# Performance work log

Hardware: AMD Instinct MI355X
Metric: run time of the kernel (lower is better)

The kernel has to match this reference:

```python
import jax, jax.numpy as jnp
import numpy as np

B, BOND, N, ATOM, UNITS = 256, 5, 128, 64, 128


def setup_inputs() -> dict:
    key = jax.random.key(0)
    k1, k2, k3 = jax.random.split(key, 3)
    adjacency = jax.random.uniform(k1, (B, BOND, N, N), dtype=jnp.float32)
    features = jax.random.normal(k2, (B, N, ATOM), dtype=jnp.float32)
    # per-sample unique kernel: (global_batch, bond_dim, atom_dim, units)
    kernel = jax.random.normal(k3, (B, BOND, ATOM, UNITS), dtype=jnp.float32) * 0.05
    return {"adjacency": adjacency, "features": features, "kernel": kernel}


def reference(adjacency, features, kernel):
    # aggregate neighbors per bond type: [B, bond, N, atom]
    x = jnp.einsum('bemn,bnd->bemd', adjacency, features)
    # per-sample, per-bond linear transform: [B, bond, N, units]
    x = jnp.einsum('bemd,bedu->bemu', x, kernel)
    # reduce over bond types, then activation: [B, N, units]
    return jax.nn.relu(jnp.sum(x, axis=1))
```

## Files before the change

### kernel.cpp

```cpp
#include <hip/hip_runtime.h>


typedef __attribute__((ext_vector_type(8))) short s8v;
typedef __attribute__((ext_vector_type(4))) float f4v;

__device__ __forceinline__ unsigned bfr(float f) {
    unsigned u = __builtin_bit_cast(unsigned, f);
    u += 0x7FFFu + ((u >> 16) & 1u);
    return u >> 16;
}
__device__ __forceinline__ unsigned pk2(float a, float b) {
    return bfr(a) | (bfr(b) << 16);
}
__device__ __forceinline__ s8v mk_frag(f4v lo, f4v hi) {
    union { unsigned u[4]; s8v s; } r;
    r.u[0] = pk2(lo[0], lo[1]); r.u[1] = pk2(lo[2], lo[3]);
    r.u[2] = pk2(hi[0], hi[1]); r.u[3] = pk2(hi[2], hi[3]);
    return r.s;
}
__device__ __forceinline__ int adrF(int d, int n) {
    return d * 128 + (((n >> 3) ^ (d & 7)) << 3) + (n & 7);
}
__device__ __forceinline__ int adrK(int u, int d) {
    return u * 64 + (((d >> 3) ^ (u & 7)) << 3) + (d & 7);
}

__global__ __launch_bounds__(256, 4)
void rgc_kernel(const float* __restrict__ adj,
                const float* __restrict__ feat,
                const float* __restrict__ ker,
                float* __restrict__ out)
{
    __shared__ __align__(16) short featT[64 * 128];
    __shared__ __align__(16) short kerT[128 * 64];
    __shared__ __align__(16) short YB[4][16 * 64];

    const int bs   = blockIdx.x & 255;
    const int Q    = blockIdx.x >> 8;
    const int tid  = threadIdx.x;
    const int w    = tid >> 6;
    const int mt   = w >> 1;
    const int uh   = w & 1;
    const int lane = tid & 63;
    const int c16  = lane & 15;
    const int quad = lane >> 4;

    const float* adjB  = adj  + (size_t)bs * (5 * 128 * 128);
    const float* featB = feat + (size_t)bs * (128 * 64);
    const float* kerB  = ker  + (size_t)bs * (5 * 64 * 128);
    float*       outB  = out  + (size_t)bs * (128 * 128);

    {
        const int sn = tid & 127, sdh = tid >> 7;
        const float* fp = featB + sn * 64 + sdh * 32;
        f4v v[8];
        #pragma unroll
        for (int i = 0; i < 8; ++i) v[i] = *(const f4v*)(fp + 4 * i);
        #pragma unroll
        for (int i = 0; i < 8; ++i)
            #pragma unroll
            for (int j = 0; j < 4; ++j) {
                const int d = 32 * sdh + 4 * i + j;
                featT[adrF(d, sn)] = (short)bfr(v[i][j]);
            }
    }
    {
        const float* kp = kerB + lane * 128 + 32 * w;
        f4v v[8];
        #pragma unroll
        for (int i = 0; i < 8; ++i) v[i] = *(const f4v*)(kp + 4 * i);
        #pragma unroll
        for (int i = 0; i < 8; ++i)
            #pragma unroll
            for (int j = 0; j < 4; ++j) {
                const int u = 32 * w + 4 * i + j;
                kerT[adrK(u, lane)] = (short)bfr(v[i][j]);
            }
    }
    __syncthreads();

    const int rowS = 32 * Q + 16 * mt;
    const float* ap0 = adjB + (rowS + c16) * 128 + 8 * quad;
    short* YBw = YB[w];

    f4v oacc[4] = {};

    for (int e = 0; e < 5; ++e) {
        const float* ap = ap0 + e * 16384;
        f4v a0[4], a1[4];
        #pragma unroll
        for (int k16 = 0; k16 < 4; ++k16) {
            a0[k16] = *(const f4v*)(ap + 32 * k16);
            a1[k16] = *(const f4v*)(ap + 32 * k16 + 4);
        }
        f4v kv[8];
        if (e < 4) {
            const float* kp = kerB + (e + 1) * 8192 + lane * 128 + 32 * w;
            #pragma unroll
            for (int i = 0; i < 8; ++i) kv[i] = *(const f4v*)(kp + 4 * i);
        }

        f4v yacc[4] = {};
        #pragma unroll
        for (int k16 = 0; k16 < 4; ++k16) {
            s8v af = mk_frag(a0[k16], a1[k16]);
            #pragma unroll
            for (int d16 = 0; d16 < 4; ++d16) {
                const int d = 16 * d16 + c16;
                s8v bf = *(const s8v*)&featT[d * 128 + (((4 * k16 + quad) ^ (d & 7)) << 3)];
                yacc[d16] = __builtin_amdgcn_mfma_f32_16x16x32_bf16(af, bf, yacc[d16], 0, 0, 0);
            }
        }

        #pragma unroll
        for (int d16 = 0; d16 < 4; ++d16)
            #pragma unroll
            for (int r = 0; r < 4; ++r) {
                const int m = 4 * quad + r;
                YBw[adrK(m, 16 * d16 + c16)] = (short)bfr(yacc[d16][r]);
            }
        s8v y0 = *(const s8v*)&YBw[c16 * 64 + ((quad ^ (c16 & 7)) << 3)];
        s8v y1 = *(const s8v*)&YBw[c16 * 64 + (((4 + quad) ^ (c16 & 7)) << 3)];

        #pragma unroll
        for (int u16 = 0; u16 < 4; ++u16) {
            const int uc = 64 * uh + 16 * u16 + c16;
            s8v b0 = *(const s8v*)&kerT[uc * 64 + ((quad ^ (uc & 7)) << 3)];
            s8v b1 = *(const s8v*)&kerT[uc * 64 + (((4 + quad) ^ (uc & 7)) << 3)];
            oacc[u16] = __builtin_amdgcn_mfma_f32_16x16x32_bf16(y0, b0, oacc[u16], 0, 0, 0);
            oacc[u16] = __builtin_amdgcn_mfma_f32_16x16x32_bf16(y1, b1, oacc[u16], 0, 0, 0);
        }

        if (e < 4) {
            __syncthreads();
            #pragma unroll
            for (int i = 0; i < 8; ++i)
                #pragma unroll
                for (int j = 0; j < 4; ++j) {
                    const int u = 32 * w + 4 * i + j;
                    kerT[adrK(u, lane)] = (short)bfr(kv[i][j]);
                }
            __syncthreads();
        }
    }

    #pragma unroll
    for (int u16 = 0; u16 < 4; ++u16)
        #pragma unroll
        for (int r = 0; r < 4; ++r)
            outB[(rowS + 4 * quad + r) * 128 + 64 * uh + 16 * u16 + c16] =
                fmaxf(oacc[u16][r], 0.f);
}

extern "C" void kernel_launch(void* const* d_in, const int* in_sizes, int n_in,
                              void* d_out, int out_size, void* d_ws, size_t ws_size,
                              hipStream_t stream)
{
    const float* adj  = (const float*)d_in[0];
    const float* feat = (const float*)d_in[1];
    const float* ker  = (const float*)d_in[2];
    rgc_kernel<<<1024, 256, 0, stream>>>(adj, feat, ker, (float*)d_out);
}
```

Baseline: 188.1 us.

## Split fused kernel into per-bond aggregation and per-sample transform kernels

Replaces the single fused kernel with two launches. The first computes adjacency×features per (bond, sample) and stores bf16 intermediates to the workspace. The second loads all five bond kernels for a column half and accumulates the transform with ReLU. This removes the redundant kernel reloads across row-quarter blocks and the per-bond barriers inside the loop. In exchange it adds workspace round-trip traffic and a second launch.

Measured after the change: 180.3 us. 1.04x faster.

```diff
diff --git a/kernel.cpp b/kernel.cpp
--- a/kernel.cpp
+++ b/kernel.cpp
@@ -21,134 +21,125 @@
 __device__ __forceinline__ int adrF(int d, int n) {
     return d * 128 + (((n >> 3) ^ (d & 7)) << 3) + (n & 7);
 }
-__device__ __forceinline__ int adrK(int u, int d) {
-    return u * 64 + (((d >> 3) ^ (u & 7)) << 3) + (d & 7);
+__device__ __forceinline__ int adrK(int r, int c) {
+    return r * 64 + (((c >> 3) ^ (r & 7)) << 3) + (c & 7);
 }
 
-__global__ __launch_bounds__(256, 4)
-void rgc_kernel(const float* __restrict__ adj,
-                const float* __restrict__ feat,
-                const float* __restrict__ ker,
-                float* __restrict__ out)
+__global__ __launch_bounds__(512, 2)
+void rgc_mm1(const float* __restrict__ adj, const float* __restrict__ feat,
+             short* __restrict__ yws)
 {
     __shared__ __align__(16) short featT[64 * 128];
-    __shared__ __align__(16) short kerT[128 * 64];
-    __shared__ __align__(16) short YB[4][16 * 64];
+    __shared__ __align__(16) short YB[8][16 * 64];
 
-    const int bs   = blockIdx.x & 255;
-    const int Q    = blockIdx.x >> 8;
-    const int tid  = threadIdx.x;
-    const int w    = tid >> 6;
-    const int mt   = w >> 1;
-    const int uh   = w & 1;
-    const int lane = tid & 63;
-    const int c16  = lane & 15;
-    const int quad = lane >> 4;
+    const int e = blockIdx.x, b = blockIdx.y;
+    const int tid = threadIdx.x;
+    const int w = tid >> 6, lane = tid & 63;
+    const int c16 = lane & 15, quad = lane >> 4;
 
-    const float* adjB  = adj  + (size_t)bs * (5 * 128 * 128);
-    const float* featB = feat + (size_t)bs * (128 * 64);
-    const float* kerB  = ker  + (size_t)bs * (5 * 64 * 128);
-    float*       outB  = out  + (size_t)bs * (128 * 128);
+    const float* adjE  = adj  + ((size_t)b * 5 + e) * 16384;
+    const float* featB = feat + (size_t)b * 8192;
 
     {
-        const int sn = tid & 127, sdh = tid >> 7;
-        const float* fp = featB + sn * 64 + sdh * 32;
-        f4v v[8];
+        const int sn = tid & 127;
+        const int dq = tid >> 7;
+        const float* fp = featB + sn * 64 + dq * 16;
+        f4v v[4];
         #pragma unroll
-        for (int i = 0; i < 8; ++i) v[i] = *(const f4v*)(fp + 4 * i);
+        for (int i = 0; i < 4; ++i) v[i] = *(const f4v*)(fp + 4 * i);
         #pragma unroll
-        for (int i = 0; i < 8; ++i)
+        for (int i = 0; i < 4; ++i)
             #pragma unroll
-            for (int j = 0; j < 4; ++j) {
-                const int d = 32 * sdh + 4 * i + j;
-                featT[adrF(d, sn)] = (short)bfr(v[i][j]);
-            }
-    }
-    {
-        const float* kp = kerB + lane * 128 + 32 * w;
-        f4v v[8];
-        #pragma unroll
-        for (int i = 0; i < 8; ++i) v[i] = *(const f4v*)(kp + 4 * i);
-        #pragma unroll
-        for (int i = 0; i < 8; ++i)
-            #pragma unroll
-            for (int j = 0; j < 4; ++j) {
-                const int u = 32 * w + 4 * i + j;
-                kerT[adrK(u, lane)] = (short)bfr(v[i][j]);
-            }
+            for (int j = 0; j < 4; ++j)
+                featT[adrF(16 * dq + 4 * i + j, sn)] = (short)bfr(v[i][j]);
     }
     __syncthreads();
 
-    const int rowS = 32 * Q + 16 * mt;
-    const float* ap0 = adjB + (rowS + c16) * 128 + 8 * quad;
+    const float* ap = adjE + (16 * w + c16) * 128 + 8 * quad;
+    f4v a0[4], a1[4];
+    #pragma unroll
+    for (int k16 = 0; k16 < 4; ++k16) {
+        a0[k16] = *(const f4v*)(ap + 32 * k16);
+        a1[k16] = *(const f4v*)(ap + 32 * k16 + 4);
+    }
+    f4v yacc[4] = {};
+    #pragma unroll
+    for (int k16 = 0; k16 < 4; ++k16) {
+        s8v af = mk_frag(a0[k16], a1[k16]);
+        #pragma unroll
+        for (int d16 = 0; d16 < 4; ++d16) {
+            const int d = 16 * d16 + c16;
+            s8v bf = *(const s8v*)&featT[d * 128 + (((4 * k16 + quad) ^ (d & 7)) << 3)];
+            yacc[d16] = __builtin_amdgcn_mfma_f32_16x16x32_bf16(af, bf, yacc[d16], 0, 0, 0);
+        }
+    }
     short* YBw = YB[w];
+    #pragma unroll
+    for (int d16 = 0; d16 < 4; ++d16)
+        #pragma unroll
+        for (int r = 0; r < 4; ++r) {
+            const int m = 4 * quad + r;
+            YBw[adrK(m, 16 * d16 + c16)] = (short)bfr(yacc[d16][r]);
+        }
+    s8v y0 = *(const s8v*)&YBw[c16 * 64 + ((quad ^ (c16 & 7)) << 3)];
+    s8v y1 = *(const s8v*)&YBw[c16 * 64 + (((4 + quad) ^ (c16 & 7)) << 3)];
+    short* yp = yws + (((size_t)b * 5 + e) * 8 + w) * 1024;
+    *(s8v*)(yp + lane * 8)       = y0;
+    *(s8v*)(yp + 512 + lane * 8) = y1;
+}
+
+__global__ __launch_bounds__(512, 2)
+void rgc_mm2(const short* __restrict__ yws, const float* __restrict__ ker,
+             float* __restrict__ out)
+{
+    __shared__ __align__(16) short kerT[5 * 64 * 64];
+
+    const int b = blockIdx.x & 255, uh = blockIdx.x >> 8;
+    const int tid = threadIdx.x;
+    const int w = tid >> 6, lane = tid & 63;
+    const int c16 = lane & 15, quad = lane >> 4;
+
+    const float* kerB  = ker + (size_t)b * 40960 + 64 * uh;
+    const short* ybase = yws + (size_t)b * 5 * 8192;
+
+    s8v y0[5], y1[5];
+    #pragma unroll
+    for (int e = 0; e < 5; ++e) {
+        const short* yp = ybase + (e * 8 + w) * 1024 + lane * 8;
+        y0[e] = *(const s8v*)yp;
+        y1[e] = *(const s8v*)(yp + 512);
+    }
+    #pragma unroll
+    for (int e = 0; e < 5; ++e) {
+        const float* kp = kerB + e * 8192 + lane * 128 + 8 * w;
+        f4v v0 = *(const f4v*)kp, v1 = *(const f4v*)(kp + 4);
+        #pragma unroll
+        for (int j = 0; j < 4; ++j)
+            kerT[e * 4096 + adrK(8 * w + j, lane)] = (short)bfr(v0[j]);
+        #pragma unroll
+        for (int j = 0; j < 4; ++j)
+            kerT[e * 4096 + adrK(8 * w + 4 + j, lane)] = (short)bfr(v1[j]);
+    }
+    __syncthreads();
 
     f4v oacc[4] = {};
-
-    for (int e = 0; e < 5; ++e) {
-        const float* ap = ap0 + e * 16384;
-        f4v a0[4], a1[4];
+    #pragma unroll
+    for (int e = 0; e < 5; ++e)
         #pragma unroll
-        for (int k16 = 0; k16 < 4; ++k16) {
-            a0[k16] = *(const f4v*)(ap + 32 * k16);
-            a1[k16] = *(const f4v*)(ap + 32 * k16 + 4);
-        }
-        f4v kv[8];
-        if (e < 4) {
-            const float* kp = kerB + (e + 1) * 8192 + lane * 128 + 32 * w;
-            #pragma unroll
-            for (int i = 0; i < 8; ++i) kv[i] = *(const f4v*)(kp + 4 * i);
+        for (int u16 = 0; u16 < 4; ++u16) {
+            const int uc = 16 * u16 + c16;
+            s8v b0 = *(const s8v*)&kerT[e * 4096 + uc * 64 + ((quad ^ (uc & 7)) << 3)];
+            s8v b1 = *(const s8v*)&kerT[e * 4096 + uc * 64 + (((4 + quad) ^ (uc & 7)) << 3)];
+            oacc[u16] = __builtin_amdgcn_mfma_f32_16x16x32_bf16(y0[e], b0, oacc[u16], 0, 0, 0);
+            oacc[u16] = __builtin_amdgcn_mfma_f32_16x16x32_bf16(y1[e], b1, oacc[u16], 0, 0, 0);
         }
 
-        f4v yacc[4] = {};
-        #pragma unroll
-        for (int k16 = 0; k16 < 4; ++k16) {
-            s8v af = mk_frag(a0[k16], a1[k16]);
-            #pragma unroll
-            for (int d16 = 0; d16 < 4; ++d16) {
-                const int d = 16 * d16 + c16;
-                s8v bf = *(const s8v*)&featT[d * 128 + (((4 * k16 + quad) ^ (d & 7)) << 3)];
-                yacc[d16] = __builtin_amdgcn_mfma_f32_16x16x32_bf16(af, bf, yacc[d16], 0, 0, 0);
-            }
-        }
-
-        #pragma unroll
-        for (int d16 = 0; d16 < 4; ++d16)
-            #pragma unroll
-            for (int r = 0; r < 4; ++r) {
-                const int m = 4 * quad + r;
-                YBw[adrK(m, 16 * d16 + c16)] = (short)bfr(yacc[d16][r]);
-            }
-        s8v y0 = *(const s8v*)&YBw[c16 * 64 + ((quad ^ (c16 & 7)) << 3)];
-        s8v y1 = *(const s8v*)&YBw[c16 * 64 + (((4 + quad) ^ (c16 & 7)) << 3)];
-
-        #pragma unroll
-        for (int u16 = 0; u16 < 4; ++u16) {
-            const int uc = 64 * uh + 16 * u16 + c16;
-            s8v b0 = *(const s8v*)&kerT[uc * 64 + ((quad ^ (uc & 7)) << 3)];
-            s8v b1 = *(const s8v*)&kerT[uc * 64 + (((4 + quad) ^ (uc & 7)) << 3)];
-            oacc[u16] = __builtin_amdgcn_mfma_f32_16x16x32_bf16(y0, b0, oacc[u16], 0, 0, 0);
-            oacc[u16] = __builtin_amdgcn_mfma_f32_16x16x32_bf16(y1, b1, oacc[u16], 0, 0, 0);
-        }
-
-        if (e < 4) {
-            __syncthreads();
-            #pragma unroll
-            for (int i = 0; i < 8; ++i)
-                #pragma unroll
-                for (int j = 0; j < 4; ++j) {
-                    const int u = 32 * w + 4 * i + j;
-                    kerT[adrK(u, lane)] = (short)bfr(kv[i][j]);
-                }
-            __syncthreads();
-        }
-    }
-
+    float* outB = out + (size_t)b * 16384;
     #pragma unroll
     for (int u16 = 0; u16 < 4; ++u16)
         #pragma unroll
         for (int r = 0; r < 4; ++r)
-            outB[(rowS + 4 * quad + r) * 128 + 64 * uh + 16 * u16 + c16] =
+            outB[(16 * w + 4 * quad + r) * 128 + 64 * uh + 16 * u16 + c16] =
                 fmaxf(oacc[u16][r], 0.f);
 }
 
@@ -159,5 +150,7 @@
     const float* adj  = (const float*)d_in[0];
     const float* feat = (const float*)d_in[1];
     const float* ker  = (const float*)d_in[2];
-    rgc_kernel<<<1024, 256, 0, stream>>>(adj, feat, ker, (float*)d_out);
+    short* yws = (short*)d_ws;
+    rgc_mm1<<<dim3(5, 256), 512, 0, stream>>>(adj, feat, yws);
+    rgc_mm2<<<512, 512, 0, stream>>>(yws, ker, (float*)d_out);
 }
```
